# Kernel optimization log

Hardware: AMD Instinct MI355X
Metric: run time of the kernel (lower is better)

Reference implementation:

```python
import jax, jax.numpy as jnp
import numpy as np

N_E = 1024
E_DIM = 64
BETA = 0.25
DECAY = 0.99
EPSILON = 1e-5


def setup_inputs() -> dict:
    key = jax.random.key(0)
    k1, k2, k3 = jax.random.split(key, 3)
    z = jax.random.normal(k1, (32, E_DIM, 32, 32), dtype=jnp.float32)
    # codebook initialized uniform(-1/n_e, 1/n_e) as in the torch module
    emb_w = jax.random.uniform(k2, (N_E, E_DIM), minval=-1.0 / N_E, maxval=1.0 / N_E, dtype=jnp.float32)
    ema_cluster_size = jnp.ones((N_E,), dtype=jnp.float32)
    ema_w = jax.random.uniform(k3, (N_E, E_DIM), minval=-1.0 / N_E, maxval=1.0 / N_E, dtype=jnp.float32)
    return {"z": z, "emb_w": emb_w, "ema_cluster_size": ema_cluster_size, "ema_w": ema_w}


def reference(z, emb_w, ema_cluster_size, ema_w):
    B, C, H, W = z.shape  # C == E_DIM
    zf = jnp.transpose(z, (0, 2, 3, 1)).reshape(-1, E_DIM)  # [N, e_dim]
    N = zf.shape[0]

    # squared-distance via ||z||^2 + ||e||^2 - 2 z.e (same expansion as torch code)
    d = (jnp.sum(zf * zf, axis=1, keepdims=True)
         + jnp.sum(emb_w * emb_w, axis=1)
         - 2.0 * zf @ emb_w.T)  # [N, n_e]
    idx = jnp.argmin(d, axis=1)  # [N]

    min_encodings = jax.nn.one_hot(idx, N_E, dtype=jnp.float32)  # [N, n_e]
    # cluster stats via scatter-add (equivalent to one-hot matmuls, cheaper)
    cluster_size = jax.ops.segment_sum(jnp.ones((N,), jnp.float32), idx, num_segments=N_E)
    sum_encodings = jax.ops.segment_sum(zf, idx, num_segments=N_E)  # [n_e, e_dim]

    # EMA update (training path, done before the z_q lookup as in torch)
    new_cs = DECAY * ema_cluster_size + (1.0 - DECAY) * cluster_size
    new_w = DECAY * ema_w + (1.0 - DECAY) * sum_encodings
    n = jnp.sum(new_cs)
    cs_norm = (new_cs + EPSILON) / (n + N_E * EPSILON) * n
    new_emb = new_w / cs_norm[:, None]  # updated codebook

    z_q = new_emb[idx].reshape(B, H, W, C).transpose(0, 3, 1, 2)  # [B,C,H,W]
    loss = BETA * jnp.mean((jax.lax.stop_gradient(z_q) - z) ** 2)
    z_q_st = z + jax.lax.stop_gradient(z_q - z)  # straight-through

    avg_probs = cluster_size / N
    perplexity = jnp.exp(-jnp.sum(avg_probs * jnp.log(avg_probs + 1e-10)))
    return loss, z_q_st, perplexity, min_encodings, idx
```

## Files before the change

### kernel.cpp

```cpp
#include <hip/hip_runtime.h>
#include <math.h>

#define NVEC 32768
#define NE   1024
#define ED   64
#define TOT  2097152
#define NCHUNK 8
#define CHUNK  128
#define MT     64

#define O_LOSS   0
#define O_ZQ     1
#define O_PERP   2097153
#define O_MINENC 2097154
#define O_IDX    35651586

#define W_PIDX   0
#define W_CS     32768
#define W_SUMENC 33792
#define W_NEWEMB 99328
#define W_ESQ    164864


__global__ void __launch_bounds__(256) k_pre(const float* __restrict__ emb,
                                             float* __restrict__ ws,
                                             float* __restrict__ out) {
    int b = blockIdx.x;
    if (b < 65) {
        int i = b * 256 + threadIdx.x;
        float4 zv; zv.x = 0.f; zv.y = 0.f; zv.z = 0.f; zv.w = 0.f;
        *(float4*)(ws + W_CS + i * 4) = zv;
        if (b == 0 && threadIdx.x == 0) out[O_LOSS] = 0.f;
    } else {
        int code = (b - 65) * 256 + threadIdx.x;
        const float* ep = emb + (size_t)code * ED;
        float r[8];
#pragma unroll
        for (int j = 0; j < 8; ++j) r[j] = __fmul_rn(ep[j], ep[j]);
#pragma unroll
        for (int i = 8; i < 64; i += 8)
#pragma unroll
            for (int j = 0; j < 8; ++j)
                r[j] = __fadd_rn(r[j], __fmul_rn(ep[i + j], ep[i + j]));
        ws[W_ESQ + code] = __fadd_rn(
            __fadd_rn(__fadd_rn(r[0], r[1]), __fadd_rn(r[2], r[3])),
            __fadd_rn(__fadd_rn(r[4], r[5]), __fadd_rn(r[6], r[7])));
    }
}

__global__ void __launch_bounds__(256, 3) k_dist(const float* __restrict__ z,
                                                 const float* __restrict__ emb,
                                                 const float* __restrict__ esq_g,
                                                 int* __restrict__ fidx,
                                                 int* __restrict__ cnt,
                                                 float* __restrict__ sumenc,
                                                 float* __restrict__ out) {
    __shared__ __align__(16) float s_a[64 * 64];
    __shared__ __align__(16) float s_b[64 * 132];
    __shared__ float s_esq[CHUNK];
    __shared__ float s_zsq[MT];
    __shared__ int s_bi[MT];

    int tid = threadIdx.x;
    int n0 = blockIdx.x * MT;
    int b = n0 >> 10, hw0 = n0 & 1023;
    const float* zb = z + b * 65536 + hw0;

#pragma unroll
    for (int j = 0; j < 4; ++j) {
        int f4i = j * 256 + tid;
        int c = f4i >> 4, pos = (f4i & 15) * 4;
        float4 v = *(const float4*)(zb + (c << 10) + pos);
        v.x = __fmul_rn(2.0f, v.x);
        v.y = __fmul_rn(2.0f, v.y);
        v.z = __fmul_rn(2.0f, v.z);
        v.w = __fmul_rn(2.0f, v.w);
        *(float4*)(s_a + c * 64 + pos) = v;
    }
    __syncthreads();

    if (tid < MT) {
        float r[8];
#pragma unroll
        for (int j = 0; j < 8; ++j) {
            float v = s_a[j * 64 + tid];
            r[j] = __fmul_rn(v, v);
        }
#pragma unroll
        for (int i = 8; i < 64; i += 8)
#pragma unroll
            for (int j = 0; j < 8; ++j) {
                float v = s_a[(i + j) * 64 + tid];
                r[j] = __fadd_rn(r[j], __fmul_rn(v, v));
            }
        s_zsq[tid] = __fmul_rn(0.25f, __fadd_rn(
            __fadd_rn(__fadd_rn(r[0], r[1]), __fadd_rn(r[2], r[3])),
            __fadd_rn(__fadd_rn(r[4], r[5]), __fadd_rn(r[6], r[7]))));
    }
    __syncthreads();

    int mi = tid & 15, ki = tid >> 4;
    int mbase = mi * 4, kbase = ki * 8;
    float zs[4];
#pragma unroll
    for (int mu = 0; mu < 4; ++mu) zs[mu] = s_zsq[mbase + mu];

    float bd[4];
    int bix[4];
#pragma unroll
    for (int mu = 0; mu < 4; ++mu) { bd[mu] = 3.4e38f; bix[mu] = kbase; }

    for (int q = 0; q < NCHUNK; ++q) {
        int k0 = q * CHUNK;
        __syncthreads();
#pragma unroll
        for (int j = 0; j < 8; ++j) {
            int f4i = j * 256 + tid;
            int kl = f4i >> 4, c4 = f4i & 15;
            float4 v = *(const float4*)(emb + (size_t)(k0 + kl) * ED + c4 * 4);
            int base = ((( kl >> 2) + c4) & 31) * 4 + (kl & 3);
            s_b[(c4 * 4 + 0) * 132 + base] = v.x;
            s_b[(c4 * 4 + 1) * 132 + base] = v.y;
            s_b[(c4 * 4 + 2) * 132 + base] = v.z;
            s_b[(c4 * 4 + 3) * 132 + base] = v.w;
        }
        if (tid < CHUNK) s_esq[tid] = esq_g[k0 + tid];
        __syncthreads();

        float acc[4][8];
#pragma unroll
        for (int mu = 0; mu < 4; ++mu)
#pragma unroll
            for (int ku = 0; ku < 8; ++ku) acc[mu][ku] = 0.f;

#pragma unroll 4
        for (int c = 0; c < 64; ++c) {
            int c4 = c >> 2;
            float4 av = *(const float4*)(s_a + c * 64 + mbase);
            float4 b0 = *(const float4*)(s_b + c * 132 + ((2 * ki + c4) & 31) * 4);
            float4 b1 = *(const float4*)(s_b + c * 132 + ((2 * ki + 1 + c4) & 31) * 4);
#pragma unroll
            for (int mu = 0; mu < 4; ++mu) {
                float a = (&av.x)[mu];
                acc[mu][0] = __fmaf_rn(a, b0.x, acc[mu][0]);
                acc[mu][1] = __fmaf_rn(a, b0.y, acc[mu][1]);
                acc[mu][2] = __fmaf_rn(a, b0.z, acc[mu][2]);
                acc[mu][3] = __fmaf_rn(a, b0.w, acc[mu][3]);
                acc[mu][4] = __fmaf_rn(a, b1.x, acc[mu][4]);
                acc[mu][5] = __fmaf_rn(a, b1.y, acc[mu][5]);
                acc[mu][6] = __fmaf_rn(a, b1.z, acc[mu][6]);
                acc[mu][7] = __fmaf_rn(a, b1.w, acc[mu][7]);
            }
        }

#pragma unroll
        for (int mu = 0; mu < 4; ++mu)
#pragma unroll
            for (int ku = 0; ku < 8; ++ku) {
                float d = __fsub_rn(__fadd_rn(zs[mu], s_esq[kbase + ku]),
                                    acc[mu][ku]);
                if (d < bd[mu]) { bd[mu] = d; bix[mu] = k0 + kbase + ku; }
            }
    }

    __syncthreads();
    float* red_d = s_b;
    int* red_i = (int*)(s_b + 1024);
#pragma unroll
    for (int mu = 0; mu < 4; ++mu) {
        red_d[ki * 64 + mbase + mu] = bd[mu];
        red_i[ki * 64 + mbase + mu] = bix[mu];
    }
    __syncthreads();
    if (tid < MT) {
        float best = red_d[tid];
        int bi = red_i[tid];
#pragma unroll
        for (int q = 1; q < 16; ++q) {
            float d = red_d[q * 64 + tid];
            int i = red_i[q * 64 + tid];
            if (d < best || (d == best && i < bi)) { best = d; bi = i; }
        }
        fidx[n0 + tid] = bi;
        out[O_IDX + n0 + tid] = (float)bi;
        s_bi[tid] = bi;
        atomicAdd(&cnt[bi], 1);
    }
    __syncthreads();

    {
        int m = tid & 63, w4 = tid >> 6;
#pragma unroll
        for (int j = 0; j < 16; ++j) {
            int c = j * 4 + w4;
            s_b[m * 65 + c] = __fmul_rn(0.5f, s_a[c * 64 + m]);
        }
    }
    __syncthreads();

    {
        int lane = tid & 63, w = tid >> 6;
#pragma unroll
        for (int t = 0; t < 16; ++t) {
            int m = (w << 4) | t;
            int bi = s_bi[m];
            float v = s_b[m * 65 + lane];
            unsafeAtomicAdd(sumenc + ((size_t)bi << 6) + lane, v);
        }
    }
}

__global__ void __launch_bounds__(1024) k_ema(const float* __restrict__ ema_cs,
                                              const float* __restrict__ ema_w,
                                              const int* __restrict__ cnt,
                                              const float* __restrict__ sumenc,
                                              float* __restrict__ newemb,
                                              float* __restrict__ out) {
    int k = threadIdx.x;
    float c = (float)cnt[k];
    float ncs = 0.99f * ema_cs[k] + (1.0f - 0.99f) * c;
    float p = c * (1.0f / (float)NVEC);
    float e = p * logf(p + 1e-10f);
    float rn_ = ncs, re_ = e;
#pragma unroll
    for (int o = 32; o > 0; o >>= 1) {
        rn_ += __shfl_down(rn_, o, 64);
        re_ += __shfl_down(re_, o, 64);
    }
    __shared__ float sn[16], se_[16];
    __shared__ float s_n;
    int wave = k >> 6, lane = k & 63;
    if (lane == 0) { sn[wave] = rn_; se_[wave] = re_; }
    __syncthreads();
    if (k == 0) {
        float tn = 0.f, te = 0.f;
#pragma unroll
        for (int w = 0; w < 16; ++w) { tn += sn[w]; te += se_[w]; }
        s_n = tn;
        out[O_PERP] = expf(-te);
    }
    __syncthreads();
    float nt = s_n;
    float csn = (ncs + 1e-5f) / (nt + 1024.0f * 1e-5f) * nt;
    __shared__ float s_csn[NE];
    s_csn[k] = csn;
    __syncthreads();
    for (int t = k; t < NE * ED; t += 1024) {
        float nw = 0.99f * ema_w[t] + (1.0f - 0.99f) * sumenc[t];
        newemb[t] = nw / s_csn[t >> 6];
    }
}

__global__ void __launch_bounds__(256) k_zq(const float* __restrict__ z,
                                            const int* __restrict__ idx,
                                            const float* __restrict__ newemb,
                                            float* __restrict__ out) {
    __shared__ int sbi[16];
    if (threadIdx.x < 16) sbi[threadIdx.x] = idx[blockIdx.x * 16 + threadIdx.x];
    __syncthreads();

    float local = 0.f;
#pragma unroll
    for (int i = 0; i < 4; ++i) {
        int t = blockIdx.x * 256 + threadIdx.x + i * 524288;
        int b = t >> 16, c = (t >> 10) & 63, hw = t & 1023;
        int n = (b << 10) | hw;
        float e = newemb[idx[n] * ED + c];
        float zv = z[t];
        float diff = e - zv;
        out[O_ZQ + t] = zv + diff;
        local = fmaf(diff, diff, local);
    }

    int t = threadIdx.x;
    int r0 = blockIdx.x * 16;
    for (int r = 0; r < 16; ++r) {
        int rbi = sbi[r];
        float* rp = out + O_MINENC + (size_t)(r0 + r) * NE;
        if (t < 254) {
            int col = 2 + t * 4;
            float4 v;
            v.x = (col == rbi) ? 1.0f : 0.0f;
            v.y = (col + 1 == rbi) ? 1.0f : 0.0f;
            v.z = (col + 2 == rbi) ? 1.0f : 0.0f;
            v.w = (col + 3 == rbi) ? 1.0f : 0.0f;
            *(float4*)(rp + col) = v;
        } else if (t == 254) {
            float2 v;
            v.x = (0 == rbi) ? 1.0f : 0.0f;
            v.y = (1 == rbi) ? 1.0f : 0.0f;
            *(float2*)(rp) = v;
        } else {
            float4 v;
            v.x = (1018 == rbi) ? 1.0f : 0.0f;
            v.y = (1019 == rbi) ? 1.0f : 0.0f;
            v.z = (1020 == rbi) ? 1.0f : 0.0f;
            v.w = (1021 == rbi) ? 1.0f : 0.0f;
            *(float4*)(rp + 1018) = v;
            float2 w;
            w.x = (1022 == rbi) ? 1.0f : 0.0f;
            w.y = (1023 == rbi) ? 1.0f : 0.0f;
            *(float2*)(rp + 1022) = w;
        }
    }

#pragma unroll
    for (int o = 32; o > 0; o >>= 1) local += __shfl_down(local, o, 64);
    __shared__ float sp[4];
    int wave = threadIdx.x >> 6;
    if ((threadIdx.x & 63) == 0) sp[wave] = local;
    __syncthreads();
    if (threadIdx.x == 0)
        unsafeAtomicAdd(out + O_LOSS,
                        ((sp[0] + sp[1]) + (sp[2] + sp[3])) * (0.25f / (float)TOT));
}

extern "C" void kernel_launch(void* const* d_in, const int* in_sizes, int n_in,
                              void* d_out, int out_size, void* d_ws, size_t ws_size,
                              hipStream_t stream) {
    const float* z      = (const float*)d_in[0];
    const float* emb    = (const float*)d_in[1];
    const float* ema_cs = (const float*)d_in[2];
    const float* ema_w  = (const float*)d_in[3];
    float* out = (float*)d_out;
    float* ws  = (float*)d_ws;

    k_pre<<<69, 256, 0, stream>>>(emb, ws, out);
    k_dist<<<512, 256, 0, stream>>>(z, emb, ws + W_ESQ, (int*)(ws + W_PIDX),
                                    (int*)(ws + W_CS), ws + W_SUMENC, out);
    k_ema<<<1, 1024, 0, stream>>>(ema_cs, ema_w, (const int*)(ws + W_CS),
                                  ws + W_SUMENC, ws + W_NEWEMB, out);
    k_zq<<<2048, 256, 0, stream>>>(z, (const int*)(ws + W_PIDX), ws + W_NEWEMB,
                                   out);
}
```

Before: 254.7 us.

## Double distance-kernel row tile to 128 with 8x8 register blocking; vectorize EMA

The distance kernel now processes 128 vectors per block instead of 64. Each thread computes an 8x8 tile of dot products, so every codebook chunk loaded into shared memory is reused across twice as many rows. The shared A layout is permuted so each thread reads two float4s per channel. The kernel grid halves to 256 blocks, which raises register and shared memory use and may lower occupancy and leave some CUs idle. Separately, the single-block EMA update loop is vectorized to float4 loads and stores.

Result: slower. 267.0 us (+4.8%).

```diff
diff --git a/kernel.cpp b/kernel.cpp
--- a/kernel.cpp
+++ b/kernel.cpp
@@ -7,7 +7,7 @@
 #define TOT  2097152
 #define NCHUNK 8
 #define CHUNK  128
-#define MT     64
+#define MT     128
 
 #define O_LOSS   0
 #define O_ZQ     1
@@ -48,14 +48,18 @@
     }
 }
 
-__global__ void __launch_bounds__(256, 3) k_dist(const float* __restrict__ z,
-                                                 const float* __restrict__ emb,
-                                                 const float* __restrict__ esq_g,
-                                                 int* __restrict__ fidx,
-                                                 int* __restrict__ cnt,
-                                                 float* __restrict__ sumenc,
-                                                 float* __restrict__ out) {
-    __shared__ __align__(16) float s_a[64 * 64];
+__device__ __forceinline__ int apos(int m) {
+    return ((m & 4) << 4) + ((m >> 3) << 2) + (m & 3);
+}
+
+__global__ void __launch_bounds__(256) k_dist(const float* __restrict__ z,
+                                              const float* __restrict__ emb,
+                                              const float* __restrict__ esq_g,
+                                              int* __restrict__ fidx,
+                                              int* __restrict__ cnt,
+                                              float* __restrict__ sumenc,
+                                              float* __restrict__ out) {
+    __shared__ __align__(16) float s_a[64 * 128];
     __shared__ __align__(16) float s_b[64 * 132];
     __shared__ float s_esq[CHUNK];
     __shared__ float s_zsq[MT];
@@ -67,30 +71,31 @@
     const float* zb = z + b * 65536 + hw0;
 
 #pragma unroll
-    for (int j = 0; j < 4; ++j) {
+    for (int j = 0; j < 8; ++j) {
         int f4i = j * 256 + tid;
-        int c = f4i >> 4, pos = (f4i & 15) * 4;
-        float4 v = *(const float4*)(zb + (c << 10) + pos);
+        int q = f4i & 31, c = f4i >> 5;
+        float4 v = *(const float4*)(zb + (c << 10) + q * 4);
         v.x = __fmul_rn(2.0f, v.x);
         v.y = __fmul_rn(2.0f, v.y);
         v.z = __fmul_rn(2.0f, v.z);
         v.w = __fmul_rn(2.0f, v.w);
-        *(float4*)(s_a + c * 64 + pos) = v;
+        *(float4*)(s_a + c * 128 + ((q & 1) << 6) + ((q >> 1) << 2)) = v;
     }
     __syncthreads();
 
     if (tid < MT) {
+        int p = apos(tid);
         float r[8];
 #pragma unroll
         for (int j = 0; j < 8; ++j) {
-            float v = s_a[j * 64 + tid];
+            float v = s_a[j * 128 + p];
             r[j] = __fmul_rn(v, v);
         }
 #pragma unroll
         for (int i = 8; i < 64; i += 8)
 #pragma unroll
             for (int j = 0; j < 8; ++j) {
-                float v = s_a[(i + j) * 64 + tid];
+                float v = s_a[(i + j) * 128 + p];
                 r[j] = __fadd_rn(r[j], __fmul_rn(v, v));
             }
         s_zsq[tid] = __fmul_rn(0.25f, __fadd_rn(
@@ -100,25 +105,25 @@
     __syncthreads();
 
     int mi = tid & 15, ki = tid >> 4;
-    int mbase = mi * 4, kbase = ki * 8;
-    float zs[4];
-#pragma unroll
-    for (int mu = 0; mu < 4; ++mu) zs[mu] = s_zsq[mbase + mu];
-
-    float bd[4];
-    int bix[4];
-#pragma unroll
-    for (int mu = 0; mu < 4; ++mu) { bd[mu] = 3.4e38f; bix[mu] = kbase; }
-
-    for (int q = 0; q < NCHUNK; ++q) {
-        int k0 = q * CHUNK;
+    int kbase = ki * 8;
+    float zs[8];
+#pragma unroll
+    for (int mu = 0; mu < 8; ++mu) zs[mu] = s_zsq[8 * mi + mu];
+
+    float bd[8];
+    int bix[8];
+#pragma unroll
+    for (int mu = 0; mu < 8; ++mu) { bd[mu] = 3.4e38f; bix[mu] = kbase; }
+
+    for (int ch = 0; ch < NCHUNK; ++ch) {
+        int k0 = ch * CHUNK;
         __syncthreads();
 #pragma unroll
         for (int j = 0; j < 8; ++j) {
             int f4i = j * 256 + tid;
             int kl = f4i >> 4, c4 = f4i & 15;
             float4 v = *(const float4*)(emb + (size_t)(k0 + kl) * ED + c4 * 4);
-            int base = ((( kl >> 2) + c4) & 31) * 4 + (kl & 3);
+            int base = (((kl >> 2) + c4) & 31) * 4 + (kl & 3);
             s_b[(c4 * 4 + 0) * 132 + base] = v.x;
             s_b[(c4 * 4 + 1) * 132 + base] = v.y;
             s_b[(c4 * 4 + 2) * 132 + base] = v.z;
@@ -127,21 +132,23 @@
         if (tid < CHUNK) s_esq[tid] = esq_g[k0 + tid];
         __syncthreads();
 
-        float acc[4][8];
-#pragma unroll
-        for (int mu = 0; mu < 4; ++mu)
+        float acc[8][8];
+#pragma unroll
+        for (int mu = 0; mu < 8; ++mu)
 #pragma unroll
             for (int ku = 0; ku < 8; ++ku) acc[mu][ku] = 0.f;
 
-#pragma unroll 4
+#pragma unroll 2
         for (int c = 0; c < 64; ++c) {
             int c4 = c >> 2;
-            float4 av = *(const float4*)(s_a + c * 64 + mbase);
+            const float* ar = s_a + c * 128 + (mi << 2);
+            float4 a0 = *(const float4*)(ar);
+            float4 a1 = *(const float4*)(ar + 64);
             float4 b0 = *(const float4*)(s_b + c * 132 + ((2 * ki + c4) & 31) * 4);
             float4 b1 = *(const float4*)(s_b + c * 132 + ((2 * ki + 1 + c4) & 31) * 4);
 #pragma unroll
-            for (int mu = 0; mu < 4; ++mu) {
-                float a = (&av.x)[mu];
+            for (int mu = 0; mu < 8; ++mu) {
+                float a = (mu < 4) ? (&a0.x)[mu] : (&a1.x)[mu - 4];
                 acc[mu][0] = __fmaf_rn(a, b0.x, acc[mu][0]);
                 acc[mu][1] = __fmaf_rn(a, b0.y, acc[mu][1]);
                 acc[mu][2] = __fmaf_rn(a, b0.z, acc[mu][2]);
@@ -154,7 +161,7 @@
         }
 
 #pragma unroll
-        for (int mu = 0; mu < 4; ++mu)
+        for (int mu = 0; mu < 8; ++mu)
 #pragma unroll
             for (int ku = 0; ku < 8; ++ku) {
                 float d = __fsub_rn(__fadd_rn(zs[mu], s_esq[kbase + ku]),
@@ -165,11 +172,11 @@
 
     __syncthreads();
     float* red_d = s_b;
-    int* red_i = (int*)(s_b + 1024);
-#pragma unroll
-    for (int mu = 0; mu < 4; ++mu) {
-        red_d[ki * 64 + mbase + mu] = bd[mu];
-        red_i[ki * 64 + mbase + mu] = bix[mu];
+    int* red_i = (int*)(s_b + 2048);
+#pragma unroll
+    for (int mu = 0; mu < 8; ++mu) {
+        red_d[ki * 128 + 8 * mi + mu] = bd[mu];
+        red_i[ki * 128 + 8 * mi + mu] = bix[mu];
     }
     __syncthreads();
     if (tid < MT) {
@@ -177,8 +184,8 @@
         int bi = red_i[tid];
 #pragma unroll
         for (int q = 1; q < 16; ++q) {
-            float d = red_d[q * 64 + tid];
-            int i = red_i[q * 64 + tid];
+            float d = red_d[q * 128 + tid];
+            int i = red_i[q * 128 + tid];
             if (d < best || (d == best && i < bi)) { best = d; bi = i; }
         }
         fidx[n0 + tid] = bi;
@@ -189,11 +196,12 @@
     __syncthreads();
 
     {
-        int m = tid & 63, w4 = tid >> 6;
-#pragma unroll
-        for (int j = 0; j < 16; ++j) {
-            int c = j * 4 + w4;
-            s_b[m * 65 + c] = __fmul_rn(0.5f, s_a[c * 64 + m]);
+        int m = tid & 127, half = tid >> 7;
+        int p = apos(m);
+#pragma unroll
+        for (int j = 0; j < 32; ++j) {
+            int c = half * 32 + j;
+            s_b[m * 65 + c] = __fmul_rn(0.5f, s_a[c * 128 + p]);
         }
     }
     __syncthreads();
@@ -201,8 +209,8 @@
     {
         int lane = tid & 63, w = tid >> 6;
 #pragma unroll
-        for (int t = 0; t < 16; ++t) {
-            int m = (w << 4) | t;
+        for (int t = 0; t < 32; ++t) {
+            int m = (w << 5) | t;
             int bi = s_bi[m];
             float v = s_b[m * 65 + lane];
             unsafeAtomicAdd(sumenc + ((size_t)bi << 6) + lane, v);
@@ -245,9 +253,21 @@
     __shared__ float s_csn[NE];
     s_csn[k] = csn;
     __syncthreads();
-    for (int t = k; t < NE * ED; t += 1024) {
-        float nw = 0.99f * ema_w[t] + (1.0f - 0.99f) * sumenc[t];
-        newemb[t] = nw / s_csn[t >> 6];
+    const float4* w4 = (const float4*)ema_w;
+    const float4* s4 = (const float4*)sumenc;
+    float4* n4 = (float4*)newemb;
+#pragma unroll 4
+    for (int it = 0; it < 16; ++it) {
+        int t4 = it * 1024 + k;
+        float4 w = w4[t4];
+        float4 s = s4[t4];
+        float cs_ = s_csn[t4 >> 4];
+        float4 o;
+        o.x = (0.99f * w.x + (1.0f - 0.99f) * s.x) / cs_;
+        o.y = (0.99f * w.y + (1.0f - 0.99f) * s.y) / cs_;
+        o.z = (0.99f * w.z + (1.0f - 0.99f) * s.z) / cs_;
+        o.w = (0.99f * w.w + (1.0f - 0.99f) * s.w) / cs_;
+        n4[t4] = o;
     }
 }
 
@@ -326,8 +346,8 @@
     float* ws  = (float*)d_ws;
 
     k_pre<<<69, 256, 0, stream>>>(emb, ws, out);
-    k_dist<<<512, 256, 0, stream>>>(z, emb, ws + W_ESQ, (int*)(ws + W_PIDX),
-                                    (int*)(ws + W_CS), ws + W_SUMENC, out);
+    k_dist<<<NVEC / MT, 256, 0, stream>>>(z, emb, ws + W_ESQ, (int*)(ws + W_PIDX),
+                                          (int*)(ws + W_CS), ws + W_SUMENC, out);
     k_ema<<<1, 1024, 0, stream>>>(ema_cs, ema_w, (const int*)(ws + W_CS),
                                   ws + W_SUMENC, ws + W_NEWEMB, out);
     k_zq<<<2048, 256, 0, stream>>>(z, (const int*)(ws + W_PIDX), ws + W_NEWEMB,
```
